# Optimization experiments

Measured on AMD Instinct MI355X. Metric: run time of the kernel, lower is better.

## Reference

```python
import jax, jax.numpy as jnp
import numpy as np

BATCH = 256
DIM = 256
ITERN = 5


def setup_inputs() -> dict:
    key = jax.random.key(0)
    g = jax.random.normal(key, (BATCH, DIM, DIM), dtype=jnp.float32)
    # Module expects SPD-like input (covariance matrices): sum of all entries
    # (= normA) must be positive. x = G G^T / dim guarantees sum(x) = ||G^T 1||^2 >= 0.
    x = jnp.matmul(g, jnp.swapaxes(g, 1, 2)) / DIM
    return {"input": x, "iterN": ITERN}


def reference(input, iterN):
    x = input
    B, d, _ = x.shape
    I3 = 3.0 * jnp.eye(d, dtype=x.dtype)  # [d, d], broadcasts over batch
    # normA = (1/3) * sum(x @ 3I) over both matrix dims == sum of all entries of x
    normA = jnp.sum(x, axis=(1, 2))  # [B]
    A = x / normA[:, None, None]

    ZY = 0.5 * (I3 - A)
    Y = jnp.matmul(A, ZY)
    Z = ZY
    if iterN < 2:
        return ZY * jnp.sqrt(normA)[:, None, None]
    # Newton-Schulz coupled iteration (strictly sequential; iterN is small & static)
    for _ in range(1, iterN - 1):
        ZY = 0.5 * jnp.matmul(I3 - Z, Y)
        Y = jnp.matmul(Y, ZY)
        Z = jnp.matmul(ZY, Z)
    ZY = jnp.matmul(jnp.matmul(0.5 * Y, I3 - Z), Y)
    y = ZY * jnp.sqrt(normA)[:, None, None]
    return y
```

## Files before the change

### kernel.cpp

```cpp
#include <hip/hip_runtime.h>


#define DD 256
#define PLN 65536
#define MATN 65536

typedef short s16x8 __attribute__((ext_vector_type(8)));
typedef short s16x4 __attribute__((ext_vector_type(4)));
typedef float f32x4 __attribute__((ext_vector_type(4)));

__device__ __forceinline__ short bf16rtn(float f) {
    unsigned u = __float_as_uint(f);
    u += 0x7FFFu + ((u >> 16) & 1u);
    return (short)(u >> 16);
}
__device__ __forceinline__ float bf16tof(short h) {
    return __uint_as_float(((unsigned)(unsigned short)h) << 16);
}

__device__ __forceinline__ void gload16(const short* g, short* l) {
    __builtin_amdgcn_global_load_lds(
        (const __attribute__((address_space(1))) void*)g,
        (__attribute__((address_space(3))) void*)l, 16, 0, 0);
}

__global__ __launch_bounds__(256) void setup_kernel(
    const float* __restrict__ x,
    short* __restrict__ zbase, int zstride,
    short* __restrict__ xbase, int xstride,
    float* __restrict__ sc)
{
    const int lb = blockIdx.x, tid = threadIdx.x;
    const float* X = x + (size_t)lb * MATN;
    short* Zh = zbase + (size_t)lb * zstride;  short* Zl = Zh + PLN;
    short* Xh = xbase + (size_t)lb * xstride;  short* Xl = Xh + PLN;
    __shared__ float red[4];
    __shared__ float sInv;

    float s = 0.f;
    for (int i = 0; i < 64; ++i) {
        const float4 v = *(const float4*)(X + ((i * 256 + tid) << 2));
        s += v.x + v.y + v.z + v.w;
    }
    for (int o = 32; o; o >>= 1) s += __shfl_down(s, o, 64);
    if ((tid & 63) == 0) red[tid >> 6] = s;
    __syncthreads();
    if (tid == 0) {
        const float t = red[0] + red[1] + red[2] + red[3];
        sc[lb] = sqrtf(t);
        sInv = 1.f / t;
    }
    __syncthreads();
    const float invN = sInv;

    for (int i = 0; i < 64; ++i) {
        const int e = (i * 256 + tid) << 2;
        const int r = e >> 8, c = e & 255;
        const float4 v = *(const float4*)(X + e);
        const float a0 = invN * v.x, a1 = invN * v.y,
                    a2 = invN * v.z, a3 = invN * v.w;
        s16x4 xh, xl, zh, zl;
        xh[0] = bf16rtn(a0); xl[0] = bf16rtn(a0 - bf16tof(xh[0]));
        xh[1] = bf16rtn(a1); xl[1] = bf16rtn(a1 - bf16tof(xh[1]));
        xh[2] = bf16rtn(a2); xl[2] = bf16rtn(a2 - bf16tof(xh[2]));
        xh[3] = bf16rtn(a3); xl[3] = bf16rtn(a3 - bf16tof(xh[3]));
        const float z0 = ((r == c + 0) ? 1.5f : 0.f) - 0.5f * a0;
        const float z1 = ((r == c + 1) ? 1.5f : 0.f) - 0.5f * a1;
        const float z2 = ((r == c + 2) ? 1.5f : 0.f) - 0.5f * a2;
        const float z3 = ((r == c + 3) ? 1.5f : 0.f) - 0.5f * a3;
        zh[0] = bf16rtn(z0); zl[0] = bf16rtn(z0 - bf16tof(zh[0]));
        zh[1] = bf16rtn(z1); zl[1] = bf16rtn(z1 - bf16tof(zh[1]));
        zh[2] = bf16rtn(z2); zl[2] = bf16rtn(z2 - bf16tof(zh[2]));
        zh[3] = bf16rtn(z3); zl[3] = bf16rtn(z3 - bf16tof(zh[3]));
        *(s16x4*)(Xh + e) = xh; *(s16x4*)(Xl + e) = xl;
        *(s16x4*)(Zh + e) = zh; *(s16x4*)(Zl + e) = zl;
    }
}

__global__ __launch_bounds__(256) void gemm_ns(
    const short* Ahg, int astride,
    const short* Bhg, int bstride,
    short* __restrict__ Chg, int cstride,
    float* __restrict__ Cfg, int cfstride,
    const float* __restrict__ sc,
    float alpha, int fold, int usesc, int nmat, int swz)
{
    __shared__ __align__(16) short sAh[4096];
    __shared__ __align__(16) short sAl[4096];
    __shared__ __align__(16) short sBh[4096];
    __shared__ __align__(16) short sBl[4096];

    const int bid = blockIdx.x;
    int lb, t;
    if (swz) {
        const int xcd = bid & 7, s = bid >> 3;
        lb = xcd * (nmat >> 3) + (s >> 2);
        t = s & 3;
    } else {
        lb = bid >> 2;
        t = bid & 3;
    }
    const int tileR = (t >> 1) << 7, tileC = (t & 1) << 7;
    const int tid = threadIdx.x, lane = tid & 63, wave = tid >> 6;
    const int wr = wave >> 1, wc = wave & 1, ln = lane & 15, quad = lane >> 4;

    const short* Ah = Ahg + (size_t)lb * astride;  const short* Al = Ah + PLN;
    const short* Bh = Bhg + (size_t)lb * bstride;  const short* Bl = Bh + PLN;

    const int srow = tid >> 2;
    const int gs = (tid & 3) ^ ((tid >> 3) & 3);
    const size_t aoff0 = (size_t)(tileR + srow) * DD + gs * 8;
    const size_t aoff1 = aoff0 + (size_t)64 * DD;
    const size_t boff0 = (size_t)(tileC + srow) * DD + gs * 8;
    const size_t boff1 = boff0 + (size_t)64 * DD;
    const int ldo0 = wave * 512;
    const int ldo1 = 2048 + wave * 512;

    f32x4 acc[4][4];
#pragma unroll
    for (int i = 0; i < 4; ++i)
#pragma unroll
        for (int j = 0; j < 4; ++j) {
            acc[i][j][0] = 0.f; acc[i][j][1] = 0.f;
            acc[i][j][2] = 0.f; acc[i][j][3] = 0.f;
        }

    const int fo = ((quad ^ ((ln >> 1) & 3)) << 3);

    for (int kt = 0; kt < DD; kt += 32) {
        __syncthreads();
        gload16(Ah + aoff0 + kt, sAh + ldo0);
        gload16(Ah + aoff1 + kt, sAh + ldo1);
        gload16(Al + aoff0 + kt, sAl + ldo0);
        gload16(Al + aoff1 + kt, sAl + ldo1);
        gload16(Bh + boff0 + kt, sBh + ldo0);
        gload16(Bh + boff1 + kt, sBh + ldo1);
        gload16(Bl + boff0 + kt, sBl + ldo0);
        gload16(Bl + boff1 + kt, sBl + ldo1);
        __syncthreads();

        s16x8 ahf[4], alf[4];
#pragma unroll
        for (int i = 0; i < 4; ++i) {
            const int ro = (wr * 64 + i * 16 + ln) * 32 + fo;
            ahf[i] = *(const s16x8*)(sAh + ro);
            alf[i] = *(const s16x8*)(sAl + ro);
        }
#pragma unroll
        for (int j = 0; j < 4; ++j) {
            const int co = (wc * 64 + j * 16 + ln) * 32 + fo;
            const s16x8 bh = *(const s16x8*)(sBh + co);
            const s16x8 bl = *(const s16x8*)(sBl + co);
#pragma unroll
            for (int i = 0; i < 4; ++i) {
                acc[i][j] = __builtin_amdgcn_mfma_f32_16x16x32_bf16(ahf[i], bh, acc[i][j], 0, 0, 0);
                acc[i][j] = __builtin_amdgcn_mfma_f32_16x16x32_bf16(alf[i], bh, acc[i][j], 0, 0, 0);
                acc[i][j] = __builtin_amdgcn_mfma_f32_16x16x32_bf16(ahf[i], bl, acc[i][j], 0, 0, 0);
            }
        }

        if (fold) {
            const int base = kt - tileR - wr * 64;
            if (0 <= base && base < 64) {
#pragma unroll
                for (int i = 0; i < 4; ++i) {
                    const int lr = i * 16 - base;
                    if (0 <= lr && lr < 32) {
#pragma unroll
                        for (int j = 0; j < 4; ++j) {
                            const int nc = wc * 64 + j * 16 + ln;
                            const int key = (nc >> 1) & 3;
#pragma unroll
                            for (int r = 0; r < 4; ++r) {
                                const int kr = lr + quad * 4 + r;
                                const int ph = nc * 32
                                    + (((kr >> 3) ^ key) << 3) + (kr & 7);
                                const float w = bf16tof(sBh[ph])
                                              + bf16tof(sBl[ph]);
                                acc[i][j][r] = fmaf(-3.0f, w, acc[i][j][r]);
                            }
                        }
                    }
                }
            }
        }
    }

    const float alphav = usesc ? sc[lb] : alpha;
    if (Chg) {
        short* Ch = Chg + (size_t)lb * cstride;  short* Cl = Ch + PLN;
#pragma unroll
        for (int i = 0; i < 4; ++i)
#pragma unroll
            for (int j = 0; j < 4; ++j) {
                const int col = tileC + wc * 64 + j * 16 + ln;
#pragma unroll
                for (int r = 0; r < 4; ++r) {
                    const int row = tileR + wr * 64 + i * 16 + quad * 4 + r;
                    const int idx = row * DD + col;
                    const float v = alphav * acc[i][j][r];
                    const short h = bf16rtn(v);
                    Ch[idx] = h;
                    Cl[idx] = bf16rtn(v - bf16tof(h));
                }
            }
    } else {
        float* Cf = Cfg + (size_t)lb * cfstride;
#pragma unroll
        for (int i = 0; i < 4; ++i)
#pragma unroll
            for (int j = 0; j < 4; ++j) {
                const int col = tileC + wc * 64 + j * 16 + ln;
#pragma unroll
                for (int r = 0; r < 4; ++r) {
                    const int row = tileR + wr * 64 + i * 16 + quad * 4 + r;
                    Cf[row * DD + col] = alphav * acc[i][j][r];
                }
            }
    }
}

extern "C" void kernel_launch(void* const* d_in, const int* in_sizes, int n_in,
                              void* d_out, int out_size, void* d_ws, size_t ws_size,
                              hipStream_t stream)
{
    const float* x = (const float*)d_in[0];
    float* out = (float*)d_out;
    const int NB = 256;

    float* sc = (float*)d_ws;
    short* base = (short*)(sc + 512);
    long availsh = (long)(ws_size / 2) - 1024;
    int nbuf = (int)(availsh / (6L * PLN));
    if (nbuf > NB) nbuf = NB;
    if (nbuf < 1) nbuf = 1;
    const int ES = 6 * PLN;
    const int EX = 2 * PLN;

    for (int c0 = 0; c0 < NB; c0 += nbuf) {
        const int n = (NB - c0 < nbuf) ? (NB - c0) : nbuf;
        const int swz = (n % 8 == 0) ? 1 : 0;
        const float* xs = x + (size_t)c0 * MATN;
        float* os = out + (size_t)c0 * MATN;
        short* XH = (short*)os;
        short* SA = base;
        short* SB = base + 2 * PLN;
        short* TT = base + 4 * PLN;
        const dim3 G(4 * n), T(256);

        setup_kernel<<<n, 256, 0, stream>>>(xs, SA, ES, XH, EX, sc);

#define GEMM_B(AH, AS, BH, BS, CH, AL, FD) \
        gemm_ns<<<G, T, 0, stream>>>((AH), (AS), (BH), (BS), (CH), ES, \
                                     nullptr, 0, sc, (AL), (FD), 0, n, swz)

        GEMM_B(XH, EX, SA, ES, SB, 1.f, 0);
        GEMM_B(SA, ES, SB, ES, TT, -0.5f, 1);
        GEMM_B(TT, ES, SA, ES, SB, 1.f, 0);
        GEMM_B(XH, EX, SB, ES, SA, 1.f, 0);
        GEMM_B(SB, ES, SA, ES, TT, -0.5f, 1);
        GEMM_B(TT, ES, SB, ES, SA, 1.f, 0);
        GEMM_B(XH, EX, SA, ES, SB, 1.f, 0);
        GEMM_B(SA, ES, SB, ES, TT, -0.5f, 1);
        GEMM_B(TT, ES, SA, ES, SB, 1.f, 0);
        GEMM_B(XH, EX, SB, ES, SA, 1.f, 0);
        GEMM_B(SB, ES, SA, ES, TT, -0.5f, 1);
        gemm_ns<<<G, T, 0, stream>>>(TT, ES, SA, ES, nullptr, 0, os, MATN,
                                     sc, 0.f, 0, 1, n, swz);
#undef GEMM_B
    }
}
```

Measured before the change: 688.7 us.

## Fuse Newton-Schulz GEMM chain into persistent cooperative kernel with per-matrix barriers

After: 1.600 ms. 132% more time.

```diff
diff --git a/kernel.cpp b/kernel.cpp
--- a/kernel.cpp
+++ b/kernel.cpp
@@ -4,6 +4,7 @@
 #define DD 256
 #define PLN 65536
 #define MATN 65536
+#define NBT 256
 
 typedef short s16x8 __attribute__((ext_vector_type(8)));
 typedef short s16x4 __attribute__((ext_vector_type(4)));
@@ -22,6 +23,11 @@
     __builtin_amdgcn_global_load_lds(
         (const __attribute__((address_space(1))) void*)g,
         (__attribute__((address_space(3))) void*)l, 16, 0, 0);
+}
+__device__ __forceinline__ void gload16c(const short* g, short* l) {
+    __builtin_amdgcn_global_load_lds(
+        (const __attribute__((address_space(1))) void*)g,
+        (__attribute__((address_space(3))) void*)l, 16, 0, 1);
 }
 
 __global__ __launch_bounds__(256) void setup_kernel(
@@ -77,6 +83,180 @@
     }
 }
 
+__global__ void init_cnt(unsigned* cnt) { cnt[threadIdx.x] = 0u; }
+
+__global__ __launch_bounds__(256, 4) void fused_chain(
+    const float* __restrict__ x, float* __restrict__ out,
+    short* __restrict__ ws, float* __restrict__ sc,
+    unsigned* __restrict__ cnt)
+{
+    __shared__ __align__(16) short sAh[4096];
+    __shared__ __align__(16) short sAl[4096];
+    __shared__ __align__(16) short sBh[4096];
+    __shared__ __align__(16) short sBl[4096];
+
+    const int bid = blockIdx.x;
+    const int xcd = bid & 7, s = bid >> 3;
+    const int lb = xcd * 32 + (s >> 2);
+    const int t = s & 3;
+    const int tileR = (t >> 1) << 7, tileC = (t & 1) << 7;
+    const int tid = threadIdx.x, lane = tid & 63, wave = tid >> 6;
+    const int wr = wave >> 1, wc = wave & 1, ln = lane & 15, quad = lane >> 4;
+
+    short* S0 = ws + (size_t)lb * (6 * (size_t)PLN);
+    short* Xp = (short*)out + (size_t)lb * (2 * (size_t)PLN);
+    float* O = out + (size_t)lb * MATN;
+
+    const int srow = tid >> 2;
+    const int gs = (tid & 3) ^ ((tid >> 3) & 3);
+    const size_t aoff0 = (size_t)(tileR + srow) * DD + gs * 8;
+    const size_t aoff1 = aoff0 + (size_t)64 * DD;
+    const size_t boff0 = (size_t)(tileC + srow) * DD + gs * 8;
+    const size_t boff1 = boff0 + (size_t)64 * DD;
+    const int ldo0 = wave * 512;
+    const int ldo1 = 2048 + wave * 512;
+    const int fo = ((quad ^ ((ln >> 1) & 3)) << 3);
+
+    constexpr unsigned SAp = 3u | (0u<<2) | (2u<<4) | (3u<<6) | (1u<<8) | (2u<<10)
+                           | (3u<<12) | (0u<<14) | (2u<<16) | (3u<<18) | (1u<<20) | (2u<<22);
+    constexpr unsigned SBp = 0u | (1u<<2) | (0u<<4) | (1u<<6) | (0u<<8) | (1u<<10)
+                           | (0u<<12) | (1u<<14) | (0u<<16) | (1u<<18) | (0u<<20) | (0u<<22);
+    constexpr unsigned SCp = 1u | (2u<<2) | (1u<<4) | (0u<<6) | (2u<<8) | (0u<<10)
+                           | (1u<<12) | (2u<<14) | (1u<<16) | (0u<<18) | (2u<<20);
+    constexpr unsigned FDm = (1u<<1) | (1u<<4) | (1u<<7) | (1u<<10);
+
+#pragma unroll 1
+    for (int st = 0; st < 12; ++st) {
+        const int sa = (SAp >> (2 * st)) & 3;
+        const int sb = (SBp >> (2 * st)) & 3;
+        const int scs = (SCp >> (2 * st)) & 3;
+        const int fold = (FDm >> st) & 1;
+        const short* Ah = (sa == 3) ? Xp : S0 + (size_t)sa * (2 * (size_t)PLN);
+        const short* Bh = (sb == 3) ? Xp : S0 + (size_t)sb * (2 * (size_t)PLN);
+        const short* Al = Ah + PLN;
+        const short* Bl = Bh + PLN;
+
+        f32x4 acc[4][4];
+#pragma unroll
+        for (int i = 0; i < 4; ++i)
+#pragma unroll
+            for (int j = 0; j < 4; ++j) {
+                acc[i][j][0] = 0.f; acc[i][j][1] = 0.f;
+                acc[i][j][2] = 0.f; acc[i][j][3] = 0.f;
+            }
+
+        for (int kt = 0; kt < DD; kt += 32) {
+            __syncthreads();
+            gload16c(Ah + aoff0 + kt, sAh + ldo0);
+            gload16c(Ah + aoff1 + kt, sAh + ldo1);
+            gload16c(Al + aoff0 + kt, sAl + ldo0);
+            gload16c(Al + aoff1 + kt, sAl + ldo1);
+            gload16c(Bh + boff0 + kt, sBh + ldo0);
+            gload16c(Bh + boff1 + kt, sBh + ldo1);
+            gload16c(Bl + boff0 + kt, sBl + ldo0);
+            gload16c(Bl + boff1 + kt, sBl + ldo1);
+            __syncthreads();
+
+            s16x8 ahf[4], alf[4];
+#pragma unroll
+            for (int i = 0; i < 4; ++i) {
+                const int ro = (wr * 64 + i * 16 + ln) * 32 + fo;
+                ahf[i] = *(const s16x8*)(sAh + ro);
+                alf[i] = *(const s16x8*)(sAl + ro);
+            }
+#pragma unroll
+            for (int j = 0; j < 4; ++j) {
+                const int co = (wc * 64 + j * 16 + ln) * 32 + fo;
+                const s16x8 bh = *(const s16x8*)(sBh + co);
+                const s16x8 bl = *(const s16x8*)(sBl + co);
+#pragma unroll
+                for (int i = 0; i < 4; ++i) {
+                    acc[i][j] = __builtin_amdgcn_mfma_f32_16x16x32_bf16(ahf[i], bh, acc[i][j], 0, 0, 0);
+                    acc[i][j] = __builtin_amdgcn_mfma_f32_16x16x32_bf16(alf[i], bh, acc[i][j], 0, 0, 0);
+                    acc[i][j] = __builtin_amdgcn_mfma_f32_16x16x32_bf16(ahf[i], bl, acc[i][j], 0, 0, 0);
+                }
+            }
+
+            if (fold) {
+                const int base = kt - tileR - wr * 64;
+                if (0 <= base && base < 64) {
+#pragma unroll
+                    for (int i = 0; i < 4; ++i) {
+                        const int lr = i * 16 - base;
+                        if (0 <= lr && lr < 32) {
+#pragma unroll
+                            for (int j = 0; j < 4; ++j) {
+                                const int nc = wc * 64 + j * 16 + ln;
+                                const int key = (nc >> 1) & 3;
+#pragma unroll
+                                for (int r = 0; r < 4; ++r) {
+                                    const int kr = lr + quad * 4 + r;
+                                    const int ph = nc * 32
+                                        + (((kr >> 3) ^ key) << 3) + (kr & 7);
+                                    const float w = bf16tof(sBh[ph])
+                                                  + bf16tof(sBl[ph]);
+                                    acc[i][j][r] = fmaf(-3.0f, w, acc[i][j][r]);
+                                }
+                            }
+                        }
+                    }
+                }
+            }
+        }
+
+        if (st == 11) {
+            unsigned su = __hip_atomic_load((unsigned*)(sc + lb),
+                                            __ATOMIC_RELAXED,
+                                            __HIP_MEMORY_SCOPE_AGENT);
+            const float alphav = __uint_as_float(su);
+#pragma unroll
+            for (int i = 0; i < 4; ++i)
+#pragma unroll
+                for (int j = 0; j < 4; ++j) {
+                    const int col = tileC + wc * 64 + j * 16 + ln;
+#pragma unroll
+                    for (int r = 0; r < 4; ++r) {
+                        const int row = tileR + wr * 64 + i * 16 + quad * 4 + r;
+                        O[row * DD + col] = alphav * acc[i][j][r];
+                    }
+                }
+        } else {
+            const float alphav = fold ? -0.5f : 1.0f;
+            short* Ch = (scs == 3) ? Xp : S0 + (size_t)scs * (2 * (size_t)PLN);
+            short* Cl = Ch + PLN;
+#pragma unroll
+            for (int i = 0; i < 4; ++i)
+#pragma unroll
+                for (int j = 0; j < 4; ++j) {
+                    const int col = tileC + wc * 64 + j * 16 + ln;
+#pragma unroll
+                    for (int r = 0; r < 4; ++r) {
+                        const int row = tileR + wr * 64 + i * 16 + quad * 4 + r;
+                        const int idx = row * DD + col;
+                        const float v = alphav * acc[i][j][r];
+                        const short h = bf16rtn(v);
+                        Ch[idx] = h;
+                        Cl[idx] = bf16rtn(v - bf16tof(h));
+                    }
+                }
+        }
+
+        __syncthreads();
+        if (tid == 0)
+            __hip_atomic_fetch_add(&cnt[lb], 1u, __ATOMIC_RELAXED,
+                                   __HIP_MEMORY_SCOPE_AGENT);
+        if (st < 11) {
+            if (tid == 0) {
+                const unsigned tgt = 4u * (unsigned)(st + 1);
+                while (__hip_atomic_load(&cnt[lb], __ATOMIC_RELAXED,
+                                         __HIP_MEMORY_SCOPE_AGENT) < tgt)
+                    __builtin_amdgcn_s_sleep(8);
+            }
+            __syncthreads();
+        }
+    }
+}
+
 __global__ __launch_bounds__(256) void gemm_ns(
     const short* Ahg, int astride,
     const short* Bhg, int bstride,
@@ -220,53 +400,74 @@
     }
 }
 
+static void run_fallback_chain(const float* xs, float* os, short* base,
+                               float* sc, int n, hipStream_t stream)
+{
+    const int ES = 6 * PLN;
+    const int EX = 2 * PLN;
+    const int swz = (n % 8 == 0) ? 1 : 0;
+    short* XH = (short*)os;
+    short* SA = base;
+    short* SB = base + 2 * PLN;
+    short* TT = base + 4 * PLN;
+    const dim3 G(4 * n), T(256);
+
+#define GEMM_B(AH, AS, BH, BS, CH, AL, FD) \
+    gemm_ns<<<G, T, 0, stream>>>((AH), (AS), (BH), (BS), (CH), ES, \
+                                 nullptr, 0, sc, (AL), (FD), 0, n, swz)
+    GEMM_B(XH, EX, SA, ES, SB, 1.f, 0);
+    GEMM_B(SA, ES, SB, ES, TT, -0.5f, 1);
+    GEMM_B(TT, ES, SA, ES, SB, 1.f, 0);
+    GEMM_B(XH, EX, SB, ES, SA, 1.f, 0);
+    GEMM_B(SB, ES, SA, ES, TT, -0.5f, 1);
+    GEMM_B(TT, ES, SB, ES, SA, 1.f, 0);
+    GEMM_B(XH, EX, SA, ES, SB, 1.f, 0);
+    GEMM_B(SA, ES, SB, ES, TT, -0.5f, 1);
+    GEMM_B(TT, ES, SA, ES, SB, 1.f, 0);
+    GEMM_B(XH, EX, SB, ES, SA, 1.f, 0);
+    GEMM_B(SB, ES, SA, ES, TT, -0.5f, 1);
+    gemm_ns<<<G, T, 0, stream>>>(TT, ES, SA, ES, nullptr, 0, os, MATN,
+                                 sc, 0.f, 0, 1, n, swz);
+#undef GEMM_B
+}
+
 extern "C" void kernel_launch(void* const* d_in, const int* in_sizes, int n_in,
                               void* d_out, int out_size, void* d_ws, size_t ws_size,
                               hipStream_t stream)
 {
     const float* x = (const float*)d_in[0];
     float* out = (float*)d_out;
-    const int NB = 256;
 
     float* sc = (float*)d_ws;
+    unsigned* cnt = (unsigned*)(sc + 256);
     short* base = (short*)(sc + 512);
     long availsh = (long)(ws_size / 2) - 1024;
     int nbuf = (int)(availsh / (6L * PLN));
-    if (nbuf > NB) nbuf = NB;
+    if (nbuf > NBT) nbuf = NBT;
     if (nbuf < 1) nbuf = 1;
     const int ES = 6 * PLN;
     const int EX = 2 * PLN;
 
-    for (int c0 = 0; c0 < NB; c0 += nbuf) {
-        const int n = (NB - c0 < nbuf) ? (NB - c0) : nbuf;
-        const int swz = (n % 8 == 0) ? 1 : 0;
-        const float* xs = x + (size_t)c0 * MATN;
-        float* os = out + (size_t)c0 * MATN;
-        short* XH = (short*)os;
-        short* SA = base;
-        short* SB = base + 2 * PLN;
-        short* TT = base + 4 * PLN;
-        const dim3 G(4 * n), T(256);
-
-        setup_kernel<<<n, 256, 0, stream>>>(xs, SA, ES, XH, EX, sc);
-
-#define GEMM_B(AH, AS, BH, BS, CH, AL, FD) \
-        gemm_ns<<<G, T, 0, stream>>>((AH), (AS), (BH), (BS), (CH), ES, \
-                                     nullptr, 0, sc, (AL), (FD), 0, n, swz)
-
-        GEMM_B(XH, EX, SA, ES, SB, 1.f, 0);
-        GEMM_B(SA, ES, SB, ES, TT, -0.5f, 1);
-        GEMM_B(TT, ES, SA, ES, SB, 1.f, 0);
-        GEMM_B(XH, EX, SB, ES, SA, 1.f, 0);
-        GEMM_B(SB, ES, SA, ES, TT, -0.5f, 1);
-        GEMM_B(TT, ES, SB, ES, SA, 1.f, 0);
-        GEMM_B(XH, EX, SA, ES, SB, 1.f, 0);
-        GEMM_B(SA, ES, SB, ES, TT, -0.5f, 1);
-        GEMM_B(TT, ES, SA, ES, SB, 1.f, 0);
-        GEMM_B(XH, EX, SB, ES, SA, 1.f, 0);
-        GEMM_B(SB, ES, SA, ES, TT, -0.5f, 1);
-        gemm_ns<<<G, T, 0, stream>>>(TT, ES, SA, ES, nullptr, 0, os, MATN,
-                                     sc, 0.f, 0, 1, n, swz);
-#undef GEMM_B
-    }
-}
+    if (nbuf >= NBT) {
+        init_cnt<<<1, 256, 0, stream>>>(cnt);
+        setup_kernel<<<NBT, 256, 0, stream>>>(x, base, ES, (short*)out, EX, sc);
+
+        const float* xa = x; float* oa = out; short* wa = base;
+        float* sca = sc; unsigned* ca = cnt;
+        void* kargs[] = {(void*)&xa, (void*)&oa, (void*)&wa,
+                         (void*)&sca, (void*)&ca};
+        hipError_t e = hipLaunchCooperativeKernel(
+            (const void*)fused_chain, dim3(8 * 128), dim3(256), kargs, 0, stream);
+        if (e != hipSuccess) {
+            run_fallback_chain(x, out, base, sc, NBT, stream);
+        }
+    } else {
+        for (int c0 = 0; c0 < NBT; c0 += nbuf) {
+            const int n = (NBT - c0 < nbuf) ? (NBT - c0) : nbuf;
+            const float* xs = x + (size_t)c0 * MATN;
+            float* os = out + (size_t)c0 * MATN;
+            setup_kernel<<<n, 256, 0, stream>>>(xs, base, ES, (short*)os, EX, sc);
+            run_fallback_chain(xs, os, base, sc, n, stream);
+        }
+    }
+}
```
